# Kernel optimization log

Measured on AMD Instinct MI355X. Metric: run time of the kernel, lower is better.

Reference implementation:

```python
import jax, jax.numpy as jnp
from jax import lax
import numpy as np

B, T, I, H, C = 4096, 2048, 1, 16, 2


def setup_inputs() -> dict:
    key = jax.random.key(0)
    ks = jax.random.split(key, 7)
    return {
        "x": jax.random.normal(ks[0], (B, T, I), dtype=jnp.float32),
        "W_ih": jax.random.normal(ks[1], (H, I), dtype=jnp.float32) * (1.0 / np.sqrt(H)),
        "b_ih": jax.random.normal(ks[2], (H,), dtype=jnp.float32) * (1.0 / np.sqrt(H)),
        "W_hh": jax.random.normal(ks[3], (H, H), dtype=jnp.float32) * (1.0 / np.sqrt(H)),
        "b_hh": jax.random.normal(ks[4], (H,), dtype=jnp.float32) * (1.0 / np.sqrt(H)),
        "W_fc": jax.random.normal(ks[5], (C, H), dtype=jnp.float32) * (1.0 / np.sqrt(H)),
        "b_fc": jax.random.normal(ks[6], (C,), dtype=jnp.float32) * (1.0 / np.sqrt(H)),
    }


def reference(x, W_ih, b_ih, W_hh, b_hh, W_fc, b_fc):
    # Precompute input contribution for all timesteps: [B, T, H]
    xi = jnp.einsum('bti,hi->bth', x, W_ih) + b_ih
    h0 = jnp.zeros((x.shape[0], W_hh.shape[0]), dtype=x.dtype)

    def step(h, xt):
        # PyTorch RNN cell (relu): h_t = relu(W_ih x_t + b_ih + W_hh h_{t-1} + b_hh)
        h = jax.nn.relu(xt + h @ W_hh.T + b_hh)
        return h, None

    hT, _ = lax.scan(step, h0, jnp.swapaxes(xi, 0, 1))  # scan over T
    # fc applied to the last timestep's hidden state (out[:, -1, :] == hT)
    return hT @ W_fc.T + b_fc
```

## Files before the change

### kernel.cpp

```cpp
#include <hip/hip_runtime.h>

#define T_LEN 2048

typedef float f4 __attribute__((ext_vector_type(4)));

__device__ __forceinline__ void step(float& h, float xi, float raw, float& xo,
                                     const float (&w)[16], float wih, float bias) {
  float a0, a1, a2, a3;
  asm("v_fma_f32 %[xo], %[raw], %[wih], %[bs]\n\t"
      "v_fma_f32 %[a0], %[h], %[w0], %[xi]\n\t"
      "v_mul_f32_dpp  %[a1], %[h], %[w1]  row_ror:1  row_mask:0xf bank_mask:0xf\n\t"
      "v_mul_f32_dpp  %[a2], %[h], %[w2]  row_ror:2  row_mask:0xf bank_mask:0xf\n\t"
      "v_mul_f32_dpp  %[a3], %[h], %[w3]  row_ror:3  row_mask:0xf bank_mask:0xf\n\t"
      "v_fmac_f32_dpp %[a0], %[h], %[w4]  row_ror:4  row_mask:0xf bank_mask:0xf\n\t"
      "v_fmac_f32_dpp %[a1], %[h], %[w5]  row_ror:5  row_mask:0xf bank_mask:0xf\n\t"
      "v_fmac_f32_dpp %[a2], %[h], %[w6]  row_ror:6  row_mask:0xf bank_mask:0xf\n\t"
      "v_fmac_f32_dpp %[a3], %[h], %[w7]  row_ror:7  row_mask:0xf bank_mask:0xf\n\t"
      "v_fmac_f32_dpp %[a0], %[h], %[w8]  row_ror:8  row_mask:0xf bank_mask:0xf\n\t"
      "v_fmac_f32_dpp %[a1], %[h], %[w9]  row_ror:9  row_mask:0xf bank_mask:0xf\n\t"
      "v_fmac_f32_dpp %[a2], %[h], %[w10] row_ror:10 row_mask:0xf bank_mask:0xf\n\t"
      "v_fmac_f32_dpp %[a3], %[h], %[w11] row_ror:11 row_mask:0xf bank_mask:0xf\n\t"
      "v_fmac_f32_dpp %[a0], %[h], %[w12] row_ror:12 row_mask:0xf bank_mask:0xf\n\t"
      "v_fmac_f32_dpp %[a1], %[h], %[w13] row_ror:13 row_mask:0xf bank_mask:0xf\n\t"
      "v_fmac_f32_dpp %[a2], %[h], %[w14] row_ror:14 row_mask:0xf bank_mask:0xf\n\t"
      "v_fmac_f32_dpp %[a3], %[h], %[w15] row_ror:15 row_mask:0xf bank_mask:0xf\n\t"
      "v_add_f32 %[a0], %[a0], %[a1]\n\t"
      "v_add_f32 %[a2], %[a2], %[a3]\n\t"
      "v_add_f32 %[a0], %[a0], %[a2]\n\t"
      "v_max_f32 %[h], 0, %[a0]"
      : [a0] "=&v"(a0), [a1] "=&v"(a1), [a2] "=&v"(a2), [a3] "=&v"(a3),
        [xo] "=&v"(xo), [h] "+v"(h)
      : [xi] "v"(xi), [raw] "v"(raw), [wih] "v"(wih), [bs] "v"(bias),
        [w0] "v"(w[0]),  [w1] "v"(w[1]),  [w2] "v"(w[2]),  [w3] "v"(w[3]),
        [w4] "v"(w[4]),  [w5] "v"(w[5]),  [w6] "v"(w[6]),  [w7] "v"(w[7]),
        [w8] "v"(w[8]),  [w9] "v"(w[9]),  [w10] "v"(w[10]), [w11] "v"(w[11]),
        [w12] "v"(w[12]), [w13] "v"(w[13]), [w14] "v"(w[14]), [w15] "v"(w[15]));
}

#define Q4(XI, RQ, XO, q)                          \
  step(h, XI[4*(q)+0], RQ[q].x, XO[4*(q)+0], w, wih, bias); \
  step(h, XI[4*(q)+1], RQ[q].y, XO[4*(q)+1], w, wih, bias); \
  step(h, XI[4*(q)+2], RQ[q].z, XO[4*(q)+2], w, wih, bias); \
  step(h, XI[4*(q)+3], RQ[q].w, XO[4*(q)+3], w, wih, bias);

#define HALF(XI, RQ, XO) \
  Q4(XI, RQ, XO, 0) Q4(XI, RQ, XO, 1) Q4(XI, RQ, XO, 2) Q4(XI, RQ, XO, 3) \
  Q4(XI, RQ, XO, 4) Q4(XI, RQ, XO, 5) Q4(XI, RQ, XO, 6) Q4(XI, RQ, XO, 7)

#define LD8(R, PS) \
  R[0] = (PS)[0]; R[1] = (PS)[1]; R[2] = (PS)[2]; R[3] = (PS)[3]; \
  R[4] = (PS)[4]; R[5] = (PS)[5]; R[6] = (PS)[6]; R[7] = (PS)[7];

__global__ __launch_bounds__(256, 1) void rnn_relu_kernel(
    const float* __restrict__ x, const float* __restrict__ W_ih,
    const float* __restrict__ b_ih, const float* __restrict__ W_hh,
    const float* __restrict__ b_hh, const float* __restrict__ W_fc,
    const float* __restrict__ b_fc, float* __restrict__ out) {
  const int tid = threadIdx.x;
  const int j   = tid & 15;
  const int b   = blockIdx.x * 16 + (tid >> 4);

  int pr = __builtin_amdgcn_update_dpp(0, j, 0x121, 0xF, 0xF, true);
  const bool plus = (pr == ((j + 1) & 15));

  float w[16];
#pragma unroll
  for (int s = 0; s < 16; ++s) {
    int k = (j + (plus ? s : (16 - s))) & 15;
    w[s] = W_hh[j * 16 + k];
  }
  const float wih  = W_ih[j];
  const float bias = b_ih[j] + b_hh[j];

  const f4* __restrict__ xr = (const f4*)(x + (size_t)b * T_LEN);

  f4 RA[8], RB[8];
  float XA[32], XB[32];
  LD8(RA, xr)
  LD8(RB, xr + 8)
#pragma unroll
  for (int i = 0; i < 8; ++i) {
    XA[4*i+0] = fmaf(RA[i].x, wih, bias);
    XA[4*i+1] = fmaf(RA[i].y, wih, bias);
    XA[4*i+2] = fmaf(RA[i].z, wih, bias);
    XA[4*i+3] = fmaf(RA[i].w, wih, bias);
  }

  float h = 0.0f;
  const f4* p2 = xr + 16;

#pragma unroll 1
  for (int k = 0; k < 64; k += 2) {
    const f4* psA = (k + 2 < 64) ? p2 : xr;
    LD8(RA, psA)
    HALF(XA, RB, XB)
    const f4* psB = (k + 3 < 64) ? (p2 + 8) : xr;
    LD8(RB, psB)
    HALF(XB, RA, XA)
    p2 += 16;
  }

  float p0 = h * W_fc[j];
  float p1 = h * W_fc[16 + j];
  p0 += __int_as_float(__builtin_amdgcn_ds_swizzle(__float_as_int(p0), 0x041F));
  p1 += __int_as_float(__builtin_amdgcn_ds_swizzle(__float_as_int(p1), 0x041F));
  p0 += __int_as_float(__builtin_amdgcn_ds_swizzle(__float_as_int(p0), 0x081F));
  p1 += __int_as_float(__builtin_amdgcn_ds_swizzle(__float_as_int(p1), 0x081F));
  p0 += __int_as_float(__builtin_amdgcn_ds_swizzle(__float_as_int(p0), 0x101F));
  p1 += __int_as_float(__builtin_amdgcn_ds_swizzle(__float_as_int(p1), 0x101F));
  p0 += __int_as_float(__builtin_amdgcn_ds_swizzle(__float_as_int(p0), 0x201F));
  p1 += __int_as_float(__builtin_amdgcn_ds_swizzle(__float_as_int(p1), 0x201F));

  if (j == 0) {
    out[b * 2 + 0] = p0 + b_fc[0];
    out[b * 2 + 1] = p1 + b_fc[1];
  }
}

extern "C" void kernel_launch(void* const* d_in, const int* in_sizes, int n_in,
                              void* d_out, int out_size, void* d_ws, size_t ws_size,
                              hipStream_t stream) {
  const float* x    = (const float*)d_in[0];
  const float* W_ih = (const float*)d_in[1];
  const float* b_ih = (const float*)d_in[2];
  const float* W_hh = (const float*)d_in[3];
  const float* b_hh = (const float*)d_in[4];
  const float* W_fc = (const float*)d_in[5];
  const float* b_fc = (const float*)d_in[6];
  float* out = (float*)d_out;

  const int B = 4096;
  dim3 grid(B / 16);
  dim3 block(256);
  hipLaunchKernelGGL(rnn_relu_kernel, grid, block, 0, stream,
                     x, W_ih, b_ih, W_hh, b_hh, W_fc, b_fc, out);
}
```

Before: 103.2 us.

## Shrink input prefetch buffers and drop occupancy-one launch bound

Replaces the 32-step double-buffered raw and precomputed input arrays with 16-step vec4 buffers and a single rolling precomputed input, so register use drops sharply. The occupancy-one launch bound is removed, letting more waves share a SIMD to hide the serial dependency latency of each recurrence step. The dot-product tree goes from four accumulators to three. In exchange, loads are issued less far ahead of use, which could expose memory latency.

```diff
diff --git a/kernel.cpp b/kernel.cpp
--- a/kernel.cpp
+++ b/kernel.cpp
@@ -4,54 +4,48 @@
 
 typedef float f4 __attribute__((ext_vector_type(4)));
 
-__device__ __forceinline__ void step(float& h, float xi, float raw, float& xo,
+__device__ __forceinline__ void step(float& h, float& xi, float xsn,
                                      const float (&w)[16], float wih, float bias) {
-  float a0, a1, a2, a3;
-  asm("v_fma_f32 %[xo], %[raw], %[wih], %[bs]\n\t"
+  float a0, a1, a2, xon;
+  asm("v_fma_f32 %[xon], %[xsn], %[wih], %[bs]\n\t"
       "v_fma_f32 %[a0], %[h], %[w0], %[xi]\n\t"
       "v_mul_f32_dpp  %[a1], %[h], %[w1]  row_ror:1  row_mask:0xf bank_mask:0xf\n\t"
       "v_mul_f32_dpp  %[a2], %[h], %[w2]  row_ror:2  row_mask:0xf bank_mask:0xf\n\t"
-      "v_mul_f32_dpp  %[a3], %[h], %[w3]  row_ror:3  row_mask:0xf bank_mask:0xf\n\t"
-      "v_fmac_f32_dpp %[a0], %[h], %[w4]  row_ror:4  row_mask:0xf bank_mask:0xf\n\t"
-      "v_fmac_f32_dpp %[a1], %[h], %[w5]  row_ror:5  row_mask:0xf bank_mask:0xf\n\t"
-      "v_fmac_f32_dpp %[a2], %[h], %[w6]  row_ror:6  row_mask:0xf bank_mask:0xf\n\t"
-      "v_fmac_f32_dpp %[a3], %[h], %[w7]  row_ror:7  row_mask:0xf bank_mask:0xf\n\t"
-      "v_fmac_f32_dpp %[a0], %[h], %[w8]  row_ror:8  row_mask:0xf bank_mask:0xf\n\t"
-      "v_fmac_f32_dpp %[a1], %[h], %[w9]  row_ror:9  row_mask:0xf bank_mask:0xf\n\t"
-      "v_fmac_f32_dpp %[a2], %[h], %[w10] row_ror:10 row_mask:0xf bank_mask:0xf\n\t"
-      "v_fmac_f32_dpp %[a3], %[h], %[w11] row_ror:11 row_mask:0xf bank_mask:0xf\n\t"
+      "v_fmac_f32_dpp %[a0], %[h], %[w3]  row_ror:3  row_mask:0xf bank_mask:0xf\n\t"
+      "v_fmac_f32_dpp %[a1], %[h], %[w4]  row_ror:4  row_mask:0xf bank_mask:0xf\n\t"
+      "v_fmac_f32_dpp %[a2], %[h], %[w5]  row_ror:5  row_mask:0xf bank_mask:0xf\n\t"
+      "v_fmac_f32_dpp %[a0], %[h], %[w6]  row_ror:6  row_mask:0xf bank_mask:0xf\n\t"
+      "v_fmac_f32_dpp %[a1], %[h], %[w7]  row_ror:7  row_mask:0xf bank_mask:0xf\n\t"
+      "v_fmac_f32_dpp %[a2], %[h], %[w8]  row_ror:8  row_mask:0xf bank_mask:0xf\n\t"
+      "v_fmac_f32_dpp %[a0], %[h], %[w9]  row_ror:9  row_mask:0xf bank_mask:0xf\n\t"
+      "v_fmac_f32_dpp %[a1], %[h], %[w10] row_ror:10 row_mask:0xf bank_mask:0xf\n\t"
+      "v_fmac_f32_dpp %[a2], %[h], %[w11] row_ror:11 row_mask:0xf bank_mask:0xf\n\t"
       "v_fmac_f32_dpp %[a0], %[h], %[w12] row_ror:12 row_mask:0xf bank_mask:0xf\n\t"
       "v_fmac_f32_dpp %[a1], %[h], %[w13] row_ror:13 row_mask:0xf bank_mask:0xf\n\t"
       "v_fmac_f32_dpp %[a2], %[h], %[w14] row_ror:14 row_mask:0xf bank_mask:0xf\n\t"
-      "v_fmac_f32_dpp %[a3], %[h], %[w15] row_ror:15 row_mask:0xf bank_mask:0xf\n\t"
+      "v_fmac_f32_dpp %[a0], %[h], %[w15] row_ror:15 row_mask:0xf bank_mask:0xf\n\t"
+      "v_add_f32 %[a1], %[a1], %[a2]\n\t"
       "v_add_f32 %[a0], %[a0], %[a1]\n\t"
-      "v_add_f32 %[a2], %[a2], %[a3]\n\t"
-      "v_add_f32 %[a0], %[a0], %[a2]\n\t"
       "v_max_f32 %[h], 0, %[a0]"
-      : [a0] "=&v"(a0), [a1] "=&v"(a1), [a2] "=&v"(a2), [a3] "=&v"(a3),
-        [xo] "=&v"(xo), [h] "+v"(h)
-      : [xi] "v"(xi), [raw] "v"(raw), [wih] "v"(wih), [bs] "v"(bias),
+      : [xon] "=&v"(xon), [a0] "=&v"(a0), [a1] "=&v"(a1), [a2] "=&v"(a2),
+        [h] "+v"(h)
+      : [xi] "v"(xi), [xsn] "v"(xsn), [wih] "v"(wih), [bs] "v"(bias),
         [w0] "v"(w[0]),  [w1] "v"(w[1]),  [w2] "v"(w[2]),  [w3] "v"(w[3]),
         [w4] "v"(w[4]),  [w5] "v"(w[5]),  [w6] "v"(w[6]),  [w7] "v"(w[7]),
         [w8] "v"(w[8]),  [w9] "v"(w[9]),  [w10] "v"(w[10]), [w11] "v"(w[11]),
         [w12] "v"(w[12]), [w13] "v"(w[13]), [w14] "v"(w[14]), [w15] "v"(w[15]));
+  xi = xon;
 }
 
-#define Q4(XI, RQ, XO, q)                          \
-  step(h, XI[4*(q)+0], RQ[q].x, XO[4*(q)+0], w, wih, bias); \
-  step(h, XI[4*(q)+1], RQ[q].y, XO[4*(q)+1], w, wih, bias); \
-  step(h, XI[4*(q)+2], RQ[q].z, XO[4*(q)+2], w, wih, bias); \
-  step(h, XI[4*(q)+3], RQ[q].w, XO[4*(q)+3], w, wih, bias);
+#define S1(XN) step(h, xi, (XN), w, wih, bias);
+#define HALF_A                                                              \
+  S1(A0.y) S1(A0.z) S1(A0.w) S1(A1.x) S1(A1.y) S1(A1.z) S1(A1.w) S1(A2.x)  \
+  S1(A2.y) S1(A2.z) S1(A2.w) S1(A3.x) S1(A3.y) S1(A3.z) S1(A3.w) S1(B0.x)
+#define HALF_B                                                              \
+  S1(B0.y) S1(B0.z) S1(B0.w) S1(B1.x) S1(B1.y) S1(B1.z) S1(B1.w) S1(B2.x)  \
+  S1(B2.y) S1(B2.z) S1(B2.w) S1(B3.x) S1(B3.y) S1(B3.z) S1(B3.w) S1(A0.x)
 
-#define HALF(XI, RQ, XO) \
-  Q4(XI, RQ, XO, 0) Q4(XI, RQ, XO, 1) Q4(XI, RQ, XO, 2) Q4(XI, RQ, XO, 3) \
-  Q4(XI, RQ, XO, 4) Q4(XI, RQ, XO, 5) Q4(XI, RQ, XO, 6) Q4(XI, RQ, XO, 7)
-
-#define LD8(R, PS) \
-  R[0] = (PS)[0]; R[1] = (PS)[1]; R[2] = (PS)[2]; R[3] = (PS)[3]; \
-  R[4] = (PS)[4]; R[5] = (PS)[5]; R[6] = (PS)[6]; R[7] = (PS)[7];
-
-__global__ __launch_bounds__(256, 1) void rnn_relu_kernel(
+__global__ __launch_bounds__(256) void rnn_relu_kernel(
     const float* __restrict__ x, const float* __restrict__ W_ih,
     const float* __restrict__ b_ih, const float* __restrict__ W_hh,
     const float* __restrict__ b_hh, const float* __restrict__ W_fc,
@@ -74,30 +68,20 @@
 
   const f4* __restrict__ xr = (const f4*)(x + (size_t)b * T_LEN);
 
-  f4 RA[8], RB[8];
-  float XA[32], XB[32];
-  LD8(RA, xr)
-  LD8(RB, xr + 8)
-#pragma unroll
-  for (int i = 0; i < 8; ++i) {
-    XA[4*i+0] = fmaf(RA[i].x, wih, bias);
-    XA[4*i+1] = fmaf(RA[i].y, wih, bias);
-    XA[4*i+2] = fmaf(RA[i].z, wih, bias);
-    XA[4*i+3] = fmaf(RA[i].w, wih, bias);
-  }
-
   float h = 0.0f;
-  const f4* p2 = xr + 16;
+  f4 A0 = xr[0], A1 = xr[1], A2 = xr[2], A3 = xr[3];
+  f4 B0, B1, B2, B3;
+  float xi = fmaf(A0.x, wih, bias);
+  const f4* p = xr + 4;
 
 #pragma unroll 1
-  for (int k = 0; k < 64; k += 2) {
-    const f4* psA = (k + 2 < 64) ? p2 : xr;
-    LD8(RA, psA)
-    HALF(XA, RB, XB)
-    const f4* psB = (k + 3 < 64) ? (p2 + 8) : xr;
-    LD8(RB, psB)
-    HALF(XB, RA, XA)
-    p2 += 16;
+  for (int t0 = 0; t0 < T_LEN; t0 += 32) {
+    B0 = p[0]; B1 = p[1]; B2 = p[2]; B3 = p[3];
+    HALF_A
+    const f4* pa = (t0 + 32 < T_LEN) ? (p + 4) : xr;
+    A0 = pa[0]; A1 = pa[1]; A2 = pa[2]; A3 = pa[3];
+    HALF_B
+    p += 8;
   }
 
   float p0 = h * W_fc[j];
```

Result: faster. 93.60 us (-9.3%).
